# Kernel optimization log

Hardware: AMD Instinct MI355X
Metric: run time of the kernel (lower is better)

The kernel has to match this reference:

```python
import jax, jax.numpy as jnp
import numpy as np

EPS = 1e-5  # BatchNorm eps; BN applied in eval mode with running_mean=0, running_var=1


def conv1x1(x, w, b=None):
    # x: [B,C,H,W], w: [O,C] -> [B,O,H,W]
    y = jnp.einsum('bchw,oc->bohw', x, w)
    if b is not None:
        y = y + b[None, :, None, None]
    return y


def bn_eval(x, gamma, beta):
    # running_mean=0, running_var=1
    scale = gamma / jnp.sqrt(1.0 + EPS)
    return x * scale[None, :, None, None] + beta[None, :, None, None]


def glnl_forward(x, mask, wt_nl, bt_nl, wp_nl, bp_nl, wt_l, bt_l, wp_l, bp_l,
                 wg_nl, bg_nl, wg_l, bg_l, wW, bW, gW, betaW, wWl, gWl, betaWl):
    B, C, H, W = x.shape
    I = wt_nl.shape[0]
    N = H * W

    # non-local branch score [B,N,N]
    th_nl = conv1x1(x, wt_nl, bt_nl).reshape(B, I, N)
    ph_nl = conv1x1(x, wp_nl, bp_nl).reshape(B, I, N)
    score_nl = jax.nn.softmax(jnp.einsum('bin,bim->bnm', th_nl, ph_nl), axis=-1)

    # local branch: mask-gated projections, score [B,N,N]
    m = mask.reshape(B, 1, N)
    th_l = conv1x1(x, wt_l, bt_l).reshape(B, I, N) * m
    ph_l = conv1x1(x, wp_l, bp_l).reshape(B, I, N) * m
    score_l = jax.nn.softmax(jnp.einsum('bin,bim->bnm', th_l, ph_l), axis=-1)

    # value projections [B,I,N]
    g_nl = conv1x1(x, wg_nl, bg_nl).reshape(B, I, N)
    g_l = conv1x1(x, wg_l, bg_l).reshape(B, I, N)

    # attention aggregation -> [B,I,H,W]
    y_nl = jnp.einsum('bnm,bim->bin', score_nl, g_nl).reshape(B, I, H, W)
    y_l = jnp.einsum('bnm,bim->bin', score_l, g_l).reshape(B, I, H, W)

    # W_local: conv1x1 (no bias) -> ReLU -> BN
    y_l = bn_eval(jax.nn.relu(conv1x1(y_l, wWl)), gWl, betaWl)

    y = y_nl + y_l
    # W: conv1x1 -> ReLU -> BN, then residual
    W_y = bn_eval(jax.nn.relu(conv1x1(y, wW, bW)), gW, betaW)
    return W_y + x


def setup_inputs() -> dict:
    key = jax.random.key(0)
    ks = jax.random.split(key, 20)
    B, C, I, H, W = 4, 128, 64, 64, 64
    s = 0.02
    inp = {
        'x': jax.random.normal(ks[0], (B, C, H, W), jnp.float32),
        'mask': (jax.random.uniform(ks[1], (B, 1, H, W)) > 0.5).astype(jnp.float32),
        'wt_nl': jax.random.normal(ks[2], (I, C)) * s, 'bt_nl': jnp.zeros((I,)),
        'wp_nl': jax.random.normal(ks[3], (I, C)) * s, 'bp_nl': jnp.zeros((I,)),
        'wt_l': jax.random.normal(ks[4], (I, C)) * s, 'bt_l': jnp.zeros((I,)),
        'wp_l': jax.random.normal(ks[5], (I, C)) * s, 'bp_l': jnp.zeros((I,)),
        'wg_nl': jax.random.normal(ks[6], (I, C)) * s, 'bg_nl': jnp.zeros((I,)),
        'wg_l': jax.random.normal(ks[7], (I, C)) * s, 'bg_l': jnp.zeros((I,)),
        'wW': jax.random.normal(ks[8], (C, I)) * s, 'bW': jnp.zeros((C,)),
        'gW': jnp.ones((C,)), 'betaW': jnp.zeros((C,)),
        'wWl': jax.random.normal(ks[9], (I, I)) * s,
        'gWl': jnp.ones((I,)), 'betaWl': jnp.zeros((I,)),
    }
    return inp


def reference(x, mask, wt_nl, bt_nl, wp_nl, bp_nl, wt_l, bt_l, wp_l, bp_l,
              wg_nl, bg_nl, wg_l, bg_l, wW, bW, gW, betaW, wWl, gWl, betaWl):
    return glnl_forward(x, mask, wt_nl, bt_nl, wp_nl, bp_nl, wt_l, bt_l, wp_l, bp_l,
                        wg_nl, bg_nl, wg_l, bg_l, wW, bW, gW, betaW, wWl, gWl, betaWl)
```

## Files before the change

### kernel.cpp

```cpp
#include <hip/hip_runtime.h>

typedef unsigned short u16;
typedef __attribute__((ext_vector_type(8))) short short8;
typedef __attribute__((ext_vector_type(4))) float floatx4;

#define MFMA16(a, b, c) __builtin_amdgcn_mfma_f32_16x16x32_bf16((a), (b), (c), 0, 0, 0)
#define LOG2E 1.44269504088896340736f

#define SZ_P ((size_t)4 * 64 * 4096)

__device__ __forceinline__ float bf2f(u16 u) {
    union { unsigned int i; float f; } v; v.i = ((unsigned int)u) << 16; return v.f;
}
__device__ __forceinline__ u16 f2bf(float f) {
    union { float f; unsigned int i; } v; v.f = f;
    unsigned int r = v.i + 0x7fffu + ((v.i >> 16) & 1u);
    return (u16)(r >> 16);
}
__device__ __forceinline__ unsigned int pk2(float a, float b) {
    union { float f; unsigned int u; } x, y; x.f = a; y.f = b;
    return (x.u >> 16) | (y.u & 0xffff0000u);
}

__global__ __launch_bounds__(256) void k_prep_w(
    const float* __restrict__ w0, const float* __restrict__ w1,
    const float* __restrict__ w2, const float* __restrict__ w3,
    const float* __restrict__ w4, const float* __restrict__ w5,
    const float* __restrict__ wWl, const float* __restrict__ wW,
    u16* __restrict__ wbf)
{
    const int idx = blockIdx.x * 256 + threadIdx.x;
    float v;
    if (idx < 49152) {
        const int j = idx >> 13, off = idx & 8191;
        const float* s = (j == 0) ? w0 : (j == 1) ? w1 : (j == 2) ? w2
                       : (j == 3) ? w3 : (j == 4) ? w4 : w5;
        v = s[off];
    } else if (idx < 53248) {
        v = wWl[idx - 49152];
    } else {
        v = wW[idx - 53248];
    }
    wbf[idx] = f2bf(v);
}

__global__ __launch_bounds__(256) void k_proj(
    const float* __restrict__ x, const float* __restrict__ mask,
    const u16* __restrict__ wbf,
    const float* __restrict__ bq0f, const float* __restrict__ bk0f,
    const float* __restrict__ bv0f,
    const float* __restrict__ bq1f, const float* __restrict__ bk1f,
    const float* __restrict__ bv1f,
    u16* __restrict__ q0, u16* __restrict__ k0, u16* __restrict__ v0,
    u16* __restrict__ q1, u16* __restrict__ k1, u16* __restrict__ v1)
{
    __shared__ __align__(16) u16 xt_s[64 * 136];
    const int n0 = blockIdx.x * 64, b = blockIdx.y;
    const int br = blockIdx.z >> 1, half = blockIdx.z & 1;
    const u16* wq = wbf + br * 24576;
    const u16* wk = wq + 8192;
    const u16* wv = wk + 8192;
    const float* bq = br ? bq1f : bq0f;
    const float* bk = br ? bk1f : bk0f;
    const float* bv = br ? bv1f : bv0f;
    u16* q = br ? q1 : q0;  u16* k = br ? k1 : k0;  u16* v = br ? v1 : v0;

    const int t = threadIdx.x, w = t >> 6, lane = t & 63;
    const int quad = lane >> 4, l15 = lane & 15;
    const float* xb = x + ((size_t)b << 19);

    for (int idx = t; idx < 8192; idx += 256) {
        const int c = idx >> 6, n = idx & 63;
        xt_s[n * 136 + c] = f2bf(xb[((size_t)c << 12) + n0 + n]);
    }
    __syncthreads();

    short8 ax[4];
#pragma unroll
    for (int cc = 0; cc < 4; ++cc)
        ax[cc] = *(const short8*)&xt_s[(w * 16 + l15) * 136 + quad * 8 + cc * 32];

    float mv[4] = {1.f, 1.f, 1.f, 1.f};
    if (br) {
#pragma unroll
        for (int r = 0; r < 4; ++r)
            mv[r] = mask[((size_t)b << 12) + n0 + w * 16 + quad * 4 + r];
    }

#pragma unroll
    for (int qk = 0; qk < 2; ++qk) {
        const u16* wsel = qk ? wk : wq;
        const float* bb = qk ? bk : bq;
        u16* o = qk ? k : q;
        const float qscale = qk ? 1.0f : LOG2E;
#pragma unroll
        for (int nsh = 0; nsh < 2; ++nsh) {
            const int ns = half * 2 + nsh;
            floatx4 acc = {0.f, 0.f, 0.f, 0.f};
            const u16* wp = wsel + (ns * 16 + l15) * 128 + quad * 8;
#pragma unroll
            for (int cc = 0; cc < 4; ++cc)
                acc = MFMA16(ax[cc], *(const short8*)(wp + cc * 32), acc);
            const float bias_i = bb[ns * 16 + l15];
#pragma unroll
            for (int r = 0; r < 4; ++r) {
                const float val = (acc[r] + bias_i) * mv[r] * qscale;
                o[((size_t)b << 18) + (size_t)(n0 + w * 16 + quad * 4 + r) * 64
                  + ns * 16 + l15] = f2bf(val);
            }
        }
    }

    short8 aw[4];
#pragma unroll
    for (int cc = 0; cc < 4; ++cc)
        aw[cc] = *(const short8*)(wv + (w * 16 + l15) * 128 + quad * 8 + cc * 32);
    float bvr[4];
#pragma unroll
    for (int r = 0; r < 4; ++r) bvr[r] = bv[w * 16 + quad * 4 + r];
#pragma unroll
    for (int nsh = 0; nsh < 2; ++nsh) {
        const int ns = half * 2 + nsh;
        floatx4 acc = {0.f, 0.f, 0.f, 0.f};
#pragma unroll
        for (int cc = 0; cc < 4; ++cc)
            acc = MFMA16(aw[cc],
                *(const short8*)&xt_s[(ns * 16 + l15) * 136 + quad * 8 + cc * 32], acc);
#pragma unroll
        for (int r = 0; r < 4; ++r) {
            v[((size_t)b << 18) + ((size_t)(w * 16 + quad * 4 + r) << 12)
              + n0 + ns * 16 + l15] = f2bf(acc[r] + bvr[r]);
        }
    }
}

__global__ __launch_bounds__(512, 4) void k_flash(
    const u16* __restrict__ Q0, const u16* __restrict__ K0,
    const u16* __restrict__ V0,
    const u16* __restrict__ Q1, const u16* __restrict__ K1,
    const u16* __restrict__ V1,
    u16* __restrict__ num, float* __restrict__ den)
{
    __shared__ __align__(16) u16 kt_s[2][64 * 72];
    __shared__ __align__(16) u16 vt_s[2][64 * 72];
    __shared__ __align__(16) u16 p_s[8 * 32 * 72];

    const int flat = blockIdx.x;
    const int g = flat & 31, tile = flat >> 5;
    const int b = g >> 3, br = (g >> 2) & 1, sp = g & 3;
    const int z = br * 4 + sp;
    const int qb = tile * 256;
    const size_t base = ((size_t)b << 18);
    const u16* Q = (br ? Q1 : Q0) + base;
    const u16* K = (br ? K1 : K0) + base;
    const u16* V = (br ? V1 : V0) + base;
    u16* numo = num + (size_t)z * SZ_P + base;
    float* deno = den + z * 16384 + b * 4096;

    const int t = threadIdx.x, w = t >> 6, lane = t & 63;
    const int quad = lane >> 4, l15 = lane & 15;
    const int pw = w * 32 * 72;

    const int r0 = t >> 3, cg8 = (t & 7) * 8;
    const u16* Kp0 = K + (size_t)r0 * 64 + cg8;
    const u16* Vp0 = V + ((size_t)r0 << 12) + cg8;
    const int lk0 = r0 * 72 + cg8;

    short8 aq[2][2];
#pragma unroll
    for (int t2 = 0; t2 < 2; ++t2)
#pragma unroll
        for (int s = 0; s < 2; ++s)
            aq[t2][s] = *(const short8*)(Q + (size_t)(qb + w * 32 + t2 * 16 + l15) * 64
                                         + s * 32 + quad * 8);

    floatx4 oacc[4][2];
#pragma unroll
    for (int it = 0; it < 4; ++it)
#pragma unroll
        for (int t2 = 0; t2 < 2; ++t2) oacc[it][t2] = (floatx4){0.f, 0.f, 0.f, 0.f};
    float dacc[2] = {0.f, 0.f};

    const int roff = tile & 15;
    const int m_beg = sp * 1024;

    {
        const int m0 = m_beg + (roff << 6);
        *(short8*)&kt_s[0][lk0] = *(const short8*)(Kp0 + (size_t)m0 * 64);
        *(short8*)&vt_s[0][lk0] = *(const short8*)(Vp0 + m0);
    }

    for (int j = 0; j < 16; ++j) {
        const int cur = j & 1;
        const int mn = m_beg + (((roff + j + 1) & 15) << 6);
        short8 pkv = *(const short8*)(Kp0 + (size_t)mn * 64);
        short8 pvv = *(const short8*)(Vp0 + mn);
        __syncthreads();

#pragma unroll
        for (int mt = 0; mt < 4; ++mt) {
            const u16* kp = &kt_s[cur][(mt * 16 + l15) * 72 + quad * 8];
            const short8 ka0 = *(const short8*)kp;
            const short8 ka1 = *(const short8*)(kp + 32);
#pragma unroll
            for (int t2 = 0; t2 < 2; ++t2) {
                floatx4 acc = {0.f, 0.f, 0.f, 0.f};
                acc = MFMA16(ka0, aq[t2][0], acc);
                acc = MFMA16(ka1, aq[t2][1], acc);
                const float e0 = exp2f(acc[0]), e1 = exp2f(acc[1]);
                const float e2 = exp2f(acc[2]), e3 = exp2f(acc[3]);
                dacc[t2] += (e0 + e1) + (e2 + e3);
                *(uint2*)&p_s[pw + (t2 * 16 + l15) * 72 + mt * 16 + quad * 4] =
                    make_uint2(pk2(e0, e1), pk2(e2, e3));
            }
        }

        short8 pb2[2][2];
#pragma unroll
        for (int t2 = 0; t2 < 2; ++t2)
#pragma unroll
            for (int s = 0; s < 2; ++s)
                pb2[t2][s] = *(const short8*)&p_s[pw + (t2 * 16 + l15) * 72 + s * 32 + quad * 8];
#pragma unroll
        for (int it = 0; it < 4; ++it) {
            const u16* vp = &vt_s[cur][(it * 16 + l15) * 72 + quad * 8];
            const short8 va0 = *(const short8*)vp;
            const short8 va1 = *(const short8*)(vp + 32);
#pragma unroll
            for (int t2 = 0; t2 < 2; ++t2) {
                oacc[it][t2] = MFMA16(va0, pb2[t2][0], oacc[it][t2]);
                oacc[it][t2] = MFMA16(va1, pb2[t2][1], oacc[it][t2]);
            }
        }

        *(short8*)&kt_s[cur ^ 1][lk0] = pkv;
        *(short8*)&vt_s[cur ^ 1][lk0] = pvv;
    }

#pragma unroll
    for (int t2 = 0; t2 < 2; ++t2) {
        float d = dacc[t2];
        d += __shfl_xor(d, 16, 64);
        d += __shfl_xor(d, 32, 64);
        if (quad == 0) deno[qb + w * 32 + t2 * 16 + l15] = d;
    }

#pragma unroll
    for (int it = 0; it < 4; ++it)
#pragma unroll
        for (int t2 = 0; t2 < 2; ++t2) {
            *(uint2*)&p_s[pw + (t2 * 16 + l15) * 72 + it * 16 + quad * 4] =
                make_uint2(pk2(oacc[it][t2][0], oacc[it][t2][1]),
                           pk2(oacc[it][t2][2], oacc[it][t2][3]));
        }
    __syncthreads();
#pragma unroll
    for (int ch = t; ch < 2048; ch += 512) {
        const int row = ch >> 3, cg = ch & 7;
        *(short8*)(numo + (size_t)(qb + row) * 64 + cg * 8) =
            *(const short8*)&p_s[(row >> 5) * 2304 + (row & 31) * 72 + cg * 8];
    }
}

__global__ __launch_bounds__(256) void k_epi(
    const u16* __restrict__ num, const float* __restrict__ den,
    const u16* __restrict__ wbf,
    const float* __restrict__ gWl, const float* __restrict__ betaWl,
    const float* __restrict__ bW, const float* __restrict__ gW,
    const float* __restrict__ betaW,
    const float* __restrict__ x, float* __restrict__ out)
{
    __shared__ __align__(16) u16 yl_s[16 * 72];
    __shared__ __align__(16) u16 ynl_s[16 * 72];
    __shared__ __align__(16) u16 yy_s[16 * 72];
    const int b = blockIdx.y, n0 = blockIdx.x * 16;
    const int t = threadIdx.x, w = t >> 6, lane = t & 63;
    const int quad = lane >> 4, l15 = lane & 15;
    const size_t ybase = ((size_t)b << 18) + (size_t)n0 * 64;

    if (t < 128) {
        const int row = t >> 3, cg = t & 7;
        float dn = 0.f, dl = 0.f;
#pragma unroll
        for (int sp = 0; sp < 4; ++sp) {
            dn += den[sp * 16384 + b * 4096 + n0 + row];
            dl += den[(4 + sp) * 16384 + b * 4096 + n0 + row];
        }
        const float inl = 1.0f / dn, ilo = 1.0f / dl;
        float an[8] = {0, 0, 0, 0, 0, 0, 0, 0}, al[8] = {0, 0, 0, 0, 0, 0, 0, 0};
#pragma unroll
        for (int sp = 0; sp < 4; ++sp) {
            const short8 vn = *(const short8*)(num + (size_t)sp * SZ_P + ybase + row * 64 + cg * 8);
            const short8 vl = *(const short8*)(num + (size_t)(4 + sp) * SZ_P + ybase + row * 64 + cg * 8);
#pragma unroll
            for (int j = 0; j < 8; ++j) {
                an[j] += bf2f((u16)vn[j]);
                al[j] += bf2f((u16)vl[j]);
            }
        }
        short8 ynl8, yl8;
#pragma unroll
        for (int j = 0; j < 8; ++j) {
            ynl8[j] = (short)f2bf(an[j] * inl);
            yl8[j]  = (short)f2bf(al[j] * ilo);
        }
        *(short8*)&ynl_s[row * 72 + cg * 8] = ynl8;
        *(short8*)&yl_s[row * 72 + cg * 8] = yl8;
    }
    __syncthreads();
    const float rsq = rsqrtf(1.0f + 1e-5f);
    const u16* wblW = wbf + 49152;
    const u16* wbW  = wbf + 53248;

    {
        const short8 a0 = *(const short8*)(wblW + (w * 16 + l15) * 64 + quad * 8);
        const short8 a1 = *(const short8*)(wblW + (w * 16 + l15) * 64 + 32 + quad * 8);
        float sc[4], bt[4];
#pragma unroll
        for (int r = 0; r < 4; ++r) {
            const int io = w * 16 + quad * 4 + r;
            sc[r] = gWl[io] * rsq;
            bt[r] = betaWl[io];
        }
        floatx4 acc = {0.f, 0.f, 0.f, 0.f};
        const u16* bp_ = &yl_s[l15 * 72 + quad * 8];
        acc = MFMA16(a0, *(const short8*)bp_, acc);
        acc = MFMA16(a1, *(const short8*)(bp_ + 32), acc);
#pragma unroll
        for (int r = 0; r < 4; ++r) {
            const int io = w * 16 + quad * 4 + r;
            float val = fmaxf(acc[r], 0.f) * sc[r] + bt[r];
            val += bf2f(ynl_s[l15 * 72 + io]);
            yy_s[l15 * 72 + io] = f2bf(val);
        }
    }
    __syncthreads();

#pragma unroll
    for (int rb = 0; rb < 2; ++rb) {
        const int c0 = rb * 64 + w * 16;
        const short8 a0 = *(const short8*)(wbW + (c0 + l15) * 64 + quad * 8);
        const short8 a1 = *(const short8*)(wbW + (c0 + l15) * 64 + 32 + quad * 8);
        float bs[4], sc[4], bt[4];
#pragma unroll
        for (int r = 0; r < 4; ++r) {
            const int c = c0 + quad * 4 + r;
            bs[r] = bW[c];
            sc[r] = gW[c] * rsq;
            bt[r] = betaW[c];
        }
        floatx4 acc = {0.f, 0.f, 0.f, 0.f};
        const u16* bp_ = &yy_s[l15 * 72 + quad * 8];
        acc = MFMA16(a0, *(const short8*)bp_, acc);
        acc = MFMA16(a1, *(const short8*)(bp_ + 32), acc);
#pragma unroll
        for (int r = 0; r < 4; ++r) {
            const int c = c0 + quad * 4 + r;
            float val = fmaxf(acc[r] + bs[r], 0.f) * sc[r] + bt[r];
            const size_t xi = ((size_t)b << 19) + ((size_t)c << 12) + n0 + l15;
            out[xi] = val + x[xi];
        }
    }
}

extern "C" void kernel_launch(void* const* d_in, const int* in_sizes, int n_in,
                              void* d_out, int out_size, void* d_ws, size_t ws_size,
                              hipStream_t stream) {
    const float* x      = (const float*)d_in[0];
    const float* mask   = (const float*)d_in[1];
    const float* wt_nl  = (const float*)d_in[2];  const float* bt_nl = (const float*)d_in[3];
    const float* wp_nl  = (const float*)d_in[4];  const float* bp_nl = (const float*)d_in[5];
    const float* wt_l   = (const float*)d_in[6];  const float* bt_l  = (const float*)d_in[7];
    const float* wp_l   = (const float*)d_in[8];  const float* bp_l  = (const float*)d_in[9];
    const float* wg_nl  = (const float*)d_in[10]; const float* bg_nl = (const float*)d_in[11];
    const float* wg_l   = (const float*)d_in[12]; const float* bg_l  = (const float*)d_in[13];
    const float* wW     = (const float*)d_in[14]; const float* bW    = (const float*)d_in[15];
    const float* gW     = (const float*)d_in[16]; const float* betaW = (const float*)d_in[17];
    const float* wWl    = (const float*)d_in[18]; const float* gWl   = (const float*)d_in[19];
    const float* betaWl = (const float*)d_in[20];

    u16* ws  = (u16*)d_ws;
    u16* wbf = ws;
    u16* q0  = wbf + 61440;
    u16* k0  = q0 + SZ_P;
    u16* v0  = k0 + SZ_P;
    u16* q1  = v0 + SZ_P;
    u16* k1  = q1 + SZ_P;
    u16* v1  = k1 + SZ_P;
    u16* num = v1 + SZ_P;
    float* den = (float*)(num + 8 * SZ_P);

    k_prep_w<<<dim3(240), 256, 0, stream>>>(wt_nl, wp_nl, wg_nl,
                                            wt_l, wp_l, wg_l, wWl, wW, wbf);
    k_proj<<<dim3(64, 4, 4), 256, 0, stream>>>(x, mask, wbf,
        bt_nl, bp_nl, bg_nl, bt_l, bp_l, bg_l,
        q0, k0, v0, q1, k1, v1);
    k_flash<<<dim3(512), 512, 0, stream>>>(q0, k0, v0, q1, k1, v1, num, den);
    k_epi<<<dim3(256, 4), 256, 0, stream>>>(num, den, wbf, gWl, betaWl,
                                            bW, gW, betaW, x, (float*)d_out);
}
```

Measured before the change: 179.4 us.

## Keep softmax probabilities in registers via permlane swaps and split keys eight ways

Attention probabilities no longer go through LDS. They are converted with the hardware bf16 pack instruction and rearranged across lanes with permlane32/16 swaps straight into the MFMA B-operand layout. This removes an LDS write/read round trip and frees shared memory, which is now one merged buffer. When the workspace is large enough, the key dimension is split into eight partials instead of four, doubling the grid to 1024 blocks for better CU occupancy. The cost is more partial num/den traffic for the epilogue to reduce, and exp2 now uses the raw hardware builtin.

Result: faster. 162.5 us (-9.4%).

```diff
diff --git a/kernel.cpp b/kernel.cpp
--- a/kernel.cpp
+++ b/kernel.cpp
@@ -3,6 +3,7 @@
 typedef unsigned short u16;
 typedef __attribute__((ext_vector_type(8))) short short8;
 typedef __attribute__((ext_vector_type(4))) float floatx4;
+typedef __attribute__((ext_vector_type(2))) unsigned int uint2e;
 
 #define MFMA16(a, b, c) __builtin_amdgcn_mfma_f32_16x16x32_bf16((a), (b), (c), 0, 0, 0)
 #define LOG2E 1.44269504088896340736f
@@ -17,9 +18,26 @@
     unsigned int r = v.i + 0x7fffu + ((v.i >> 16) & 1u);
     return (u16)(r >> 16);
 }
-__device__ __forceinline__ unsigned int pk2(float a, float b) {
-    union { float f; unsigned int u; } x, y; x.f = a; y.f = b;
-    return (x.u >> 16) | (y.u & 0xffff0000u);
+__device__ __forceinline__ unsigned int cvtpk(float a, float b) {
+    unsigned int r;
+    asm("v_cvt_pk_bf16_f32 %0, %1, %2" : "=v"(r) : "v"(a), "v"(b));
+    return r;
+}
+__device__ __forceinline__ void plswap32(unsigned int &a, unsigned int &b) {
+#if __has_builtin(__builtin_amdgcn_permlane32_swap)
+    uint2e r = __builtin_amdgcn_permlane32_swap(a, b, false, false);
+    a = r.x; b = r.y;
+#else
+    asm volatile("v_permlane32_swap_b32 %0, %1" : "+v"(a), "+v"(b));
+#endif
+}
+__device__ __forceinline__ void plswap16(unsigned int &a, unsigned int &b) {
+#if __has_builtin(__builtin_amdgcn_permlane16_swap)
+    uint2e r = __builtin_amdgcn_permlane16_swap(a, b, false, false);
+    a = r.x; b = r.y;
+#else
+    asm volatile("v_permlane16_swap_b32 %0, %1" : "+v"(a), "+v"(b));
+#endif
 }
 
 __global__ __launch_bounds__(256) void k_prep_w(
@@ -134,6 +152,7 @@
     }
 }
 
+template<int NSP>
 __global__ __launch_bounds__(512, 4) void k_flash(
     const u16* __restrict__ Q0, const u16* __restrict__ K0,
     const u16* __restrict__ V0,
@@ -141,14 +160,15 @@
     const u16* __restrict__ V1,
     u16* __restrict__ num, float* __restrict__ den)
 {
-    __shared__ __align__(16) u16 kt_s[2][64 * 72];
-    __shared__ __align__(16) u16 vt_s[2][64 * 72];
-    __shared__ __align__(16) u16 p_s[8 * 32 * 72];
+    constexpr int NIT = 4096 / NSP / 64;
+    constexpr int SPB = (NSP == 4) ? 2 : 3;
+
+    __shared__ __align__(16) u16 smem[18432];
 
     const int flat = blockIdx.x;
-    const int g = flat & 31, tile = flat >> 5;
-    const int b = g >> 3, br = (g >> 2) & 1, sp = g & 3;
-    const int z = br * 4 + sp;
+    const int g = flat & ((1 << (SPB + 3)) - 1), tile = flat >> (SPB + 3);
+    const int b = g >> (SPB + 1), br = (g >> SPB) & 1, sp = g & (NSP - 1);
+    const int z = br * NSP + sp;
     const int qb = tile * 256;
     const size_t base = ((size_t)b << 18);
     const u16* Q = (br ? Q1 : Q0) + base;
@@ -181,60 +201,78 @@
         for (int t2 = 0; t2 < 2; ++t2) oacc[it][t2] = (floatx4){0.f, 0.f, 0.f, 0.f};
     float dacc[2] = {0.f, 0.f};
 
-    const int roff = tile & 15;
-    const int m_beg = sp * 1024;
+    const int roff = tile & (NIT - 1);
+    const int m_beg = sp * (4096 / NSP);
 
     {
         const int m0 = m_beg + (roff << 6);
-        *(short8*)&kt_s[0][lk0] = *(const short8*)(Kp0 + (size_t)m0 * 64);
-        *(short8*)&vt_s[0][lk0] = *(const short8*)(Vp0 + m0);
-    }
-
-    for (int j = 0; j < 16; ++j) {
+        *(short8*)&smem[lk0] = *(const short8*)(Kp0 + (size_t)m0 * 64);
+        *(short8*)&smem[9216 + lk0] = *(const short8*)(Vp0 + m0);
+    }
+
+    for (int j = 0; j < NIT; ++j) {
         const int cur = j & 1;
-        const int mn = m_beg + (((roff + j + 1) & 15) << 6);
-        short8 pkv = *(const short8*)(Kp0 + (size_t)mn * 64);
-        short8 pvv = *(const short8*)(Vp0 + mn);
+        const u16* kt = smem + cur * 4608;
+        const u16* vt = smem + 9216 + cur * 4608;
+        short8 pkv, pvv;
+        const bool pf = (j + 1 < NIT);
+        if (pf) {
+            const int mn = m_beg + (((roff + j + 1) & (NIT - 1)) << 6);
+            pkv = *(const short8*)(Kp0 + (size_t)mn * 64);
+            pvv = *(const short8*)(Vp0 + mn);
+        }
         __syncthreads();
 
 #pragma unroll
-        for (int mt = 0; mt < 4; ++mt) {
-            const u16* kp = &kt_s[cur][(mt * 16 + l15) * 72 + quad * 8];
-            const short8 ka0 = *(const short8*)kp;
-            const short8 ka1 = *(const short8*)(kp + 32);
+        for (int s = 0; s < 2; ++s) {
+            unsigned int w0[2][2], w1[2][2];
+#pragma unroll
+            for (int mtl = 0; mtl < 2; ++mtl) {
+                const int mt = s * 2 + mtl;
+                const u16* kp = kt + (mt * 16 + l15) * 72 + quad * 8;
+                const short8 ka0 = *(const short8*)kp;
+                const short8 ka1 = *(const short8*)(kp + 32);
+#pragma unroll
+                for (int t2 = 0; t2 < 2; ++t2) {
+                    floatx4 acc = {0.f, 0.f, 0.f, 0.f};
+                    acc = MFMA16(ka0, aq[t2][0], acc);
+                    acc = MFMA16(ka1, aq[t2][1], acc);
+                    const float e0 = __builtin_amdgcn_exp2f(acc[0]);
+                    const float e1 = __builtin_amdgcn_exp2f(acc[1]);
+                    const float e2 = __builtin_amdgcn_exp2f(acc[2]);
+                    const float e3 = __builtin_amdgcn_exp2f(acc[3]);
+                    dacc[t2] += (e0 + e1) + (e2 + e3);
+                    w0[mtl][t2] = cvtpk(e0, e1);
+                    w1[mtl][t2] = cvtpk(e2, e3);
+                }
+            }
+            short8 pb[2];
 #pragma unroll
             for (int t2 = 0; t2 < 2; ++t2) {
-                floatx4 acc = {0.f, 0.f, 0.f, 0.f};
-                acc = MFMA16(ka0, aq[t2][0], acc);
-                acc = MFMA16(ka1, aq[t2][1], acc);
-                const float e0 = exp2f(acc[0]), e1 = exp2f(acc[1]);
-                const float e2 = exp2f(acc[2]), e3 = exp2f(acc[3]);
-                dacc[t2] += (e0 + e1) + (e2 + e3);
-                *(uint2*)&p_s[pw + (t2 * 16 + l15) * 72 + mt * 16 + quad * 4] =
-                    make_uint2(pk2(e0, e1), pk2(e2, e3));
+                unsigned int a0 = w0[0][t2], b0 = w0[1][t2];
+                unsigned int a1 = w1[0][t2], b1 = w1[1][t2];
+                plswap32(a0, b0); plswap16(a0, b0);
+                plswap32(a1, b1); plswap16(a1, b1);
+                union { unsigned int u[4]; short8 s8; } cv;
+                cv.u[0] = a0; cv.u[1] = a1; cv.u[2] = b0; cv.u[3] = b1;
+                pb[t2] = cv.s8;
             }
-        }
-
-        short8 pb2[2][2];
-#pragma unroll
-        for (int t2 = 0; t2 < 2; ++t2)
-#pragma unroll
-            for (int s = 0; s < 2; ++s)
-                pb2[t2][s] = *(const short8*)&p_s[pw + (t2 * 16 + l15) * 72 + s * 32 + quad * 8];
-#pragma unroll
-        for (int it = 0; it < 4; ++it) {
-            const u16* vp = &vt_s[cur][(it * 16 + l15) * 72 + quad * 8];
-            const short8 va0 = *(const short8*)vp;
-            const short8 va1 = *(const short8*)(vp + 32);
-#pragma unroll
-            for (int t2 = 0; t2 < 2; ++t2) {
-                oacc[it][t2] = MFMA16(va0, pb2[t2][0], oacc[it][t2]);
-                oacc[it][t2] = MFMA16(va1, pb2[t2][1], oacc[it][t2]);
+#pragma unroll
+            for (int it = 0; it < 4; ++it) {
+                const short8 va = *(const short8*)(vt + (it * 16 + l15) * 72
+                                                  + s * 32 + quad * 8);
+#pragma unroll
+                for (int t2 = 0; t2 < 2; ++t2)
+                    oacc[it][t2] = MFMA16(va, pb[t2], oacc[it][t2]);
             }
         }
 
-        *(short8*)&kt_s[cur ^ 1][lk0] = pkv;
-        *(short8*)&vt_s[cur ^ 1][lk0] = pvv;
+        if (pf) {
+            u16* ktn = smem + (cur ^ 1) * 4608;
+            u16* vtn = smem + 9216 + (cur ^ 1) * 4608;
+            *(short8*)&ktn[lk0] = pkv;
+            *(short8*)&vtn[lk0] = pvv;
+        }
     }
 
 #pragma unroll
@@ -245,23 +283,25 @@
         if (quad == 0) deno[qb + w * 32 + t2 * 16 + l15] = d;
     }
 
+    __syncthreads();
 #pragma unroll
     for (int it = 0; it < 4; ++it)
 #pragma unroll
         for (int t2 = 0; t2 < 2; ++t2) {
-            *(uint2*)&p_s[pw + (t2 * 16 + l15) * 72 + it * 16 + quad * 4] =
-                make_uint2(pk2(oacc[it][t2][0], oacc[it][t2][1]),
-                           pk2(oacc[it][t2][2], oacc[it][t2][3]));
+            *(uint2*)&smem[pw + (t2 * 16 + l15) * 72 + it * 16 + quad * 4] =
+                make_uint2(cvtpk(oacc[it][t2][0], oacc[it][t2][1]),
+                           cvtpk(oacc[it][t2][2], oacc[it][t2][3]));
         }
     __syncthreads();
 #pragma unroll
     for (int ch = t; ch < 2048; ch += 512) {
         const int row = ch >> 3, cg = ch & 7;
         *(short8*)(numo + (size_t)(qb + row) * 64 + cg * 8) =
-            *(const short8*)&p_s[(row >> 5) * 2304 + (row & 31) * 72 + cg * 8];
-    }
-}
-
+            *(const short8*)&smem[(row >> 5) * 2304 + (row & 31) * 72 + cg * 8];
+    }
+}
+
+template<int NSP>
 __global__ __launch_bounds__(256) void k_epi(
     const u16* __restrict__ num, const float* __restrict__ den,
     const u16* __restrict__ wbf,
@@ -282,16 +322,16 @@
         const int row = t >> 3, cg = t & 7;
         float dn = 0.f, dl = 0.f;
 #pragma unroll
-        for (int sp = 0; sp < 4; ++sp) {
+        for (int sp = 0; sp < NSP; ++sp) {
             dn += den[sp * 16384 + b * 4096 + n0 + row];
-            dl += den[(4 + sp) * 16384 + b * 4096 + n0 + row];
+            dl += den[(NSP + sp) * 16384 + b * 4096 + n0 + row];
         }
         const float inl = 1.0f / dn, ilo = 1.0f / dl;
         float an[8] = {0, 0, 0, 0, 0, 0, 0, 0}, al[8] = {0, 0, 0, 0, 0, 0, 0, 0};
 #pragma unroll
-        for (int sp = 0; sp < 4; ++sp) {
+        for (int sp = 0; sp < NSP; ++sp) {
             const short8 vn = *(const short8*)(num + (size_t)sp * SZ_P + ybase + row * 64 + cg * 8);
-            const short8 vl = *(const short8*)(num + (size_t)(4 + sp) * SZ_P + ybase + row * 64 + cg * 8);
+            const short8 vl = *(const short8*)(num + (size_t)(NSP + sp) * SZ_P + ybase + row * 64 + cg * 8);
 #pragma unroll
             for (int j = 0; j < 8; ++j) {
                 an[j] += bf2f((u16)vn[j]);
@@ -379,6 +419,10 @@
     const float* wWl    = (const float*)d_in[18]; const float* gWl   = (const float*)d_in[19];
     const float* betaWl = (const float*)d_in[20];
 
+    const size_t need8 = ((size_t)61440 + 6 * SZ_P + 16 * SZ_P) * 2
+                       + (size_t)16 * 16384 * 4;
+    const int nsp = (ws_size >= need8) ? 8 : 4;
+
     u16* ws  = (u16*)d_ws;
     u16* wbf = ws;
     u16* q0  = wbf + 61440;
@@ -388,14 +432,20 @@
     u16* k1  = q1 + SZ_P;
     u16* v1  = k1 + SZ_P;
     u16* num = v1 + SZ_P;
-    float* den = (float*)(num + 8 * SZ_P);
+    float* den = (float*)(num + (size_t)2 * nsp * SZ_P);
 
     k_prep_w<<<dim3(240), 256, 0, stream>>>(wt_nl, wp_nl, wg_nl,
                                             wt_l, wp_l, wg_l, wWl, wW, wbf);
     k_proj<<<dim3(64, 4, 4), 256, 0, stream>>>(x, mask, wbf,
         bt_nl, bp_nl, bg_nl, bt_l, bp_l, bg_l,
         q0, k0, v0, q1, k1, v1);
-    k_flash<<<dim3(512), 512, 0, stream>>>(q0, k0, v0, q1, k1, v1, num, den);
-    k_epi<<<dim3(256, 4), 256, 0, stream>>>(num, den, wbf, gWl, betaWl,
-                                            bW, gW, betaW, x, (float*)d_out);
-}
+    if (nsp == 8) {
+        k_flash<8><<<dim3(1024), 512, 0, stream>>>(q0, k0, v0, q1, k1, v1, num, den);
+        k_epi<8><<<dim3(256, 4), 256, 0, stream>>>(num, den, wbf, gWl, betaWl,
+                                                   bW, gW, betaW, x, (float*)d_out);
+    } else {
+        k_flash<4><<<dim3(512), 512, 0, stream>>>(q0, k0, v0, q1, k1, v1, num, den);
+        k_epi<4><<<dim3(256, 4), 256, 0, stream>>>(num, den, wbf, gWl, betaWl,
+                                                   bW, gW, betaW, x, (float*)d_out);
+    }
+}
```
